# Kernel optimization log

Hardware: AMD Instinct MI355X
Metric: run time of the kernel (lower is better)

## Reference

```python
import jax, jax.numpy as jnp
import numpy as np

B, C, H, W = 8, 384, 32, 32
NH, DK, DV = 8, 48, 48
CFF = 4 * C
L = H * W
NBIAS = (2 * H - 1) * (2 * W - 1)
LN_EPS = 1e-5


def _relative_indices(height, width):
    # rel_idx[q, k] = (gy_k - gy_q + H) * W + (gx_k - gx_q + W), matching the torch loop
    gy, gx = np.meshgrid(np.arange(height), np.arange(width), indexing='ij')
    gy = gy.ravel(); gx = gx.ravel()
    rel = (gy[None, :] - gy[:, None] + height) * width + (gx[None, :] - gx[:, None] + width)
    return jnp.asarray(rel, dtype=jnp.int64)


def setup_inputs() -> dict:
    key = jax.random.key(0)
    ks = jax.random.split(key, 10)
    s = 0.02  # small init scale
    return {
        'x': jax.random.normal(ks[0], (B, C, H, W), dtype=jnp.float32),
        'gamma': jnp.ones((C,), jnp.float32),
        'beta': jnp.zeros((C,), jnp.float32),
        'Wq': jax.random.normal(ks[1], (NH * DK, C), jnp.float32) * s,
        'Wk': jax.random.normal(ks[2], (NH * DK, C), jnp.float32) * s,
        'Wv': jax.random.normal(ks[3], (NH * DV, C), jnp.float32) * s,
        'Wo': jax.random.normal(ks[4], (C, NH * DV), jnp.float32) * s,
        'bo': jnp.zeros((C,), jnp.float32),
        'rel_bias': jax.random.normal(ks[5], (NH, NBIAS), jnp.float32),
        'fc1_w': jax.random.normal(ks[6], (CFF, C), jnp.float32) * s,
        'fc1_b': jnp.zeros((CFF,), jnp.float32),
        'fc2_w': jax.random.normal(ks[7], (C, CFF), jnp.float32) * s,
        'fc2_b': jnp.zeros((C,), jnp.float32),
        'rel_idx': _relative_indices(H, W),
    }


def reference(x, gamma, beta, Wq, Wk, Wv, Wo, bo, rel_bias,
              fc1_w, fc1_b, fc2_w, fc2_b, rel_idx):
    b, c, h_sp, w_sp = x.shape
    l = h_sp * w_sp
    nh = rel_bias.shape[0]
    dk = Wq.shape[0] // nh
    dv = Wv.shape[0] // nh

    # LayerNorm over channel dim (NHWC), then flatten to tokens [b, l, c]
    t = jnp.transpose(x, (0, 2, 3, 1))
    mu = jnp.mean(t, axis=-1, keepdims=True)
    var = jnp.mean(jnp.square(t - mu), axis=-1, keepdims=True)
    t = (t - mu) / jnp.sqrt(var + LN_EPS) * gamma + beta
    tok = t.reshape(b, l, c)

    q = (tok @ Wq.T).reshape(b, l, nh, dk)
    k = (tok @ Wk.T).reshape(b, l, nh, dk)
    v = (tok @ Wv.T).reshape(b, l, nh, dv)

    # gathered relative position bias: [nh, l, l]
    bias = rel_bias[:, rel_idx]
    # note: original applies NO 1/sqrt(d_k) scaling
    scores = jnp.einsum('blhd,bmhd->bhlm', q, k) + bias[None]
    attn = jax.nn.softmax(scores, axis=-1)
    out = jnp.einsum('bhlm,bmhd->blhd', attn, v).reshape(b, l, nh * dv)
    out = out @ Wo.T + bo  # [b, l, c]
    out = jnp.transpose(out, (0, 2, 1)).reshape(b, c, h_sp, w_sp)

    y = x + out  # attention residual (x_stem = x, no downsampling)

    # FFN: 1x1 convs == per-pixel linear over channels; exact (erf) gelu as torch default
    u = jnp.einsum('bchw,oc->bohw', y, fc1_w) + fc1_b[None, :, None, None]
    u = jax.nn.gelu(u, approximate=False)
    u = jnp.einsum('bchw,oc->bohw', u, fc2_w) + fc2_b[None, :, None, None]
    return y + u
```

## Files before the change

kernel.cpp:

```cpp
#include <hip/hip_runtime.h>
#include <math.h>

#define SL 1024
#define CH 384
#define NHEAD 8
#define DH 48
#define NBIAS 3969
#define NTOK 8192
#define BATCH 8
#define CFF 1536
#define LN_EPS 1e-5f
#define QKVLD 1152
#define HMS 3145728
#define LOG2E 1.4426950408889634f

#define WQKV_OFF 0
#define WO_OFF   442368
#define F1_OFF   589824
#define F2_OFF   1179648
#define WTOT     1769472

typedef float floatx4 __attribute__((ext_vector_type(4)));
typedef short bf16x8 __attribute__((ext_vector_type(8)));

__device__ __forceinline__ unsigned f2bf_u(float f) {
  unsigned u = __float_as_uint(f);
  return (u + 0x7fffu + ((u >> 16) & 1u)) >> 16;
}
__device__ __forceinline__ unsigned pack2(float a, float b) {
  return f2bf_u(a) | (f2bf_u(b) << 16);
}

__device__ __forceinline__ void gload_lds16(const void* g, void* l) {
  __builtin_amdgcn_global_load_lds(
      (const __attribute__((address_space(1))) void*)g,
      (__attribute__((address_space(3))) void*)l, 16, 0, 0);
}

__global__ void k_w2bf(const float* __restrict__ Wq, const float* __restrict__ Wk,
                       const float* __restrict__ Wv, const float* __restrict__ Wo,
                       const float* __restrict__ f1, const float* __restrict__ f2,
                       short* __restrict__ dst) {
  size_t i = ((size_t)blockIdx.x * 256 + threadIdx.x) * 8;
  if (i >= WTOT) return;
  const float* s;
  size_t base;
  if (i < 147456)        { s = Wq; base = 0; }
  else if (i < 294912)   { s = Wk; base = 147456; }
  else if (i < WO_OFF)   { s = Wv; base = 294912; }
  else if (i < F1_OFF)   { s = Wo; base = WO_OFF; }
  else if (i < F2_OFF)   { s = f1; base = F1_OFF; }
  else                   { s = f2; base = F2_OFF; }
  const float4* p = (const float4*)(s + (i - base));
  float4 a = p[0], b = p[1];
  uint4 o;
  o.x = pack2(a.x, a.y); o.y = pack2(a.z, a.w);
  o.z = pack2(b.x, b.y); o.w = pack2(b.z, b.w);
  *(uint4*)(dst + i) = o;
}

__global__ __launch_bounds__(256) void k_ln_fused(
    const float* __restrict__ x, const float* __restrict__ gamma,
    const float* __restrict__ beta, short* __restrict__ tok) {
  __shared__ float sx[32][385];
  int b = blockIdx.y, l0 = blockIdx.x * 32;
  int tid = threadIdx.x;
  const float* xb = x + (size_t)b * CH * SL;
  int cr = tid >> 3, ls = (tid & 7) * 4;
#pragma unroll
  for (int c0 = 0; c0 < CH; c0 += 32) {
    int c = c0 + cr;
    float4 v = *(const float4*)(xb + (size_t)c * SL + l0 + ls);
    sx[ls + 0][c] = v.x; sx[ls + 1][c] = v.y;
    sx[ls + 2][c] = v.z; sx[ls + 3][c] = v.w;
  }
  __syncthreads();
  int tl = tid >> 3, p = tid & 7;
  float vals[48];
  float s = 0.f, q = 0.f;
#pragma unroll
  for (int i = 0; i < 48; i++) {
    float v = sx[tl][p * 48 + i];
    vals[i] = v; s += v; q += v * v;
  }
  s += __shfl_xor(s, 1, 64); q += __shfl_xor(q, 1, 64);
  s += __shfl_xor(s, 2, 64); q += __shfl_xor(q, 2, 64);
  s += __shfl_xor(s, 4, 64); q += __shfl_xor(q, 4, 64);
  float mu = s * (1.0f / CH);
  float rstd = rsqrtf(q * (1.0f / CH) - mu * mu + LN_EPS);
  short* orow = tok + (size_t)(b * SL + l0 + tl) * CH + p * 48;
#pragma unroll
  for (int i = 0; i < 48; i += 2) {
    float a = (vals[i] - mu) * rstd * gamma[p * 48 + i] + beta[p * 48 + i];
    float c = (vals[i + 1] - mu) * rstd * gamma[p * 48 + i + 1] + beta[p * 48 + i + 1];
    *(unsigned*)(orow + i) = pack2(a, c);
  }
}

template <int BM, bool GELU, bool HAS_BIAS, int RES_MODE, int OUT_MODE>
__global__ __launch_bounds__(256) void k_gemm_mfma(
    const short* __restrict__ A, const short* __restrict__ W,
    const float* __restrict__ bias, const float* __restrict__ res,
    float* __restrict__ Cf, short* __restrict__ Cb, float* __restrict__ Ct,
    short* __restrict__ Chm, int N, int K) {
  constexpr int MI = BM / 32;
  constexpr int ASI = BM * 2 / 64;
  __shared__ short As[BM * 64];
  __shared__ short Bs[128 * 64];
  int tid = threadIdx.x;
  int wid = tid >> 6, lane = tid & 63;
  int lanelo = lane & 15, quad = lane >> 4;
  int wm = wid & 1, wn = wid >> 1;
  int m0 = blockIdx.y * BM, n0 = blockIdx.x * 128;

  const short* Aga[ASI];
  short* Ala[ASI];
#pragma unroll
  for (int s = 0; s < ASI; s++) {
    int p = wid * (BM * 2) + s * 64 + lane;
    int row = p >> 3, ch = (p & 7) ^ (row & 7);
    Aga[s] = A + (size_t)(m0 + row) * K + ch * 8;
    Ala[s] = As + (wid * (BM * 2) + s * 64) * 8;
  }
  const short* Bga[4];
  short* Bla[4];
#pragma unroll
  for (int s = 0; s < 4; s++) {
    int p = wid * 256 + s * 64 + lane;
    int row = p >> 3, ch = (p & 7) ^ (row & 7);
    Bga[s] = W + (size_t)(n0 + row) * K + ch * 8;
    Bla[s] = Bs + (wid * 256 + s * 64) * 8;
  }

  floatx4 acc[MI][4];
#pragma unroll
  for (int i = 0; i < MI; i++)
#pragma unroll
    for (int j = 0; j < 4; j++) acc[i][j] = {0.f, 0.f, 0.f, 0.f};

  int x8 = lanelo & 7;
  int ca0 = (quad ^ x8) * 8;
  int ca1 = ((quad + 4) ^ x8) * 8;

  for (int k0 = 0; k0 < K; k0 += 64) {
    __syncthreads();
#pragma unroll
    for (int s = 0; s < ASI; s++) gload_lds16(Aga[s] + k0, Ala[s]);
#pragma unroll
    for (int s = 0; s < 4; s++) gload_lds16(Bga[s] + k0, Bla[s]);
    __syncthreads();
#pragma unroll
    for (int h = 0; h < 2; h++) {
      int co = h ? ca1 : ca0;
      bf16x8 af[MI], bq[4];
#pragma unroll
      for (int i = 0; i < MI; i++)
        af[i] = *(const bf16x8*)&As[(wm * (BM / 2) + i * 16 + lanelo) * 64 + co];
#pragma unroll
      for (int j = 0; j < 4; j++)
        bq[j] = *(const bf16x8*)&Bs[(wn * 64 + j * 16 + lanelo) * 64 + co];
#pragma unroll
      for (int i = 0; i < MI; i++)
#pragma unroll
        for (int j = 0; j < 4; j++)
          acc[i][j] = __builtin_amdgcn_mfma_f32_16x16x32_bf16(af[i], bq[j], acc[i][j], 0, 0, 0);
    }
  }

  int colb = n0 + wn * 64 + lanelo;
  float bvv[4];
#pragma unroll
  for (int j = 0; j < 4; j++) bvv[j] = HAS_BIAS ? bias[colb + j * 16] : 0.0f;
#pragma unroll
  for (int i = 0; i < MI; i++) {
    int r = m0 + wm * (BM / 2) + i * 16 + quad * 4;
    int bb = r >> 10, ll = r & 1023;
#pragma unroll
    for (int j = 0; j < 4; j++) {
      int c = colb + j * 16;
      float4 rv = {0.f, 0.f, 0.f, 0.f};
      if (RES_MODE == 2) rv = *(const float4*)(res + ((size_t)bb * CH + c) * SL + ll);
      float vv[4];
#pragma unroll
      for (int reg = 0; reg < 4; reg++) {
        float v = acc[i][j][reg] + bvv[j];
        if (RES_MODE == 1) v += res[(size_t)(r + reg) * N + c];
        if (RES_MODE == 2) v += (&rv.x)[reg];
        if (GELU) v = 0.5f * v * (1.0f + erff(v * 0.7071067811865476f));
        vv[reg] = v;
      }
      if (OUT_MODE & 1) {
#pragma unroll
        for (int reg = 0; reg < 4; reg++) Cf[(size_t)(r + reg) * N + c] = vv[reg];
      }
      if (OUT_MODE & 2) {
#pragma unroll
        for (int reg = 0; reg < 4; reg++) Cb[(size_t)(r + reg) * N + c] = (short)f2bf_u(vv[reg]);
      }
      if (OUT_MODE & 4) {
        float4 ov = {vv[0], vv[1], vv[2], vv[3]};
        *(float4*)(Ct + ((size_t)bb * CH + c) * SL + ll) = ov;
      }
      if (OUT_MODE & 8) {
        int part = c / 384;
        int rem = c - part * 384;
        int hh = rem / 48, dd = rem - hh * 48;
        short* dst = Chm + (size_t)part * HMS +
                     ((size_t)(bb * NHEAD + hh) * SL + ll) * 48 + dd;
#pragma unroll
        for (int reg = 0; reg < 4; reg++) dst[reg * 48] = (short)f2bf_u(vv[reg]);
      }
    }
  }
}

__global__ __launch_bounds__(256) void k_attn_mfma(
    const short* __restrict__ qh, const short* __restrict__ kh,
    const short* __restrict__ vh, const float* __restrict__ rel_bias,
    short* __restrict__ ao) {
  __shared__ short QP[128 * 72];
  __shared__ short Ks[64 * 72];
  __shared__ short Vts[48 * 72];
  __shared__ float Bb[1152];

  int b = blockIdx.z, h = blockIdx.y;
  int l0 = blockIdx.x * 128;
  int tid = threadIdx.x;
  int wid = tid >> 6, lane = tid & 63;
  int lanelo = lane & 15, quad = lane >> 4;
  size_t hb = ((size_t)b * NHEAD + h) * SL;
  size_t bSL = (size_t)b * SL;
  const short* kbase = kh + hb * 48;
  const short* vbase = vh + hb * 48;

  {
    const short* qsrc = qh + (hb + l0) * 48;
#pragma unroll
    for (int s = 0; s < 3; s++) {
      int g = tid + 256 * s;
      int row = g / 6, pos = g - row * 6;
      *(uint4*)&QP[row * 72 + pos * 8] = *(const uint4*)(qsrc + g * 8);
    }
  }
  {
    const float* bsrc = rel_bias + h * NBIAS + (929 - l0);
    for (int j = tid; j < 1152; j += 256) Bb[j] = bsrc[j] * LOG2E;
  }
  for (int z = tid; z < 128 * 8; z += 256) {
    int r = z >> 3, u = z & 7;
    ((unsigned*)&QP[r * 72 + 48])[u] = 0u;
    if (r < 64) ((unsigned*)&Ks[r * 72 + 48])[u] = 0u;
  }
  __syncthreads();

  bf16x8 aq[2][2];
#pragma unroll
  for (int qi = 0; qi < 2; qi++) {
    aq[qi][0] = *(const bf16x8*)&QP[(wid * 32 + qi * 16 + lanelo) * 72 + quad * 8];
    aq[qi][1] = *(const bf16x8*)&QP[(wid * 32 + qi * 16 + lanelo) * 72 + 32 + quad * 8];
  }

  floatx4 O[3][2];
#pragma unroll
  for (int dt = 0; dt < 3; dt++)
#pragma unroll
    for (int qi = 0; qi < 2; qi++) O[dt][qi] = {0.f, 0.f, 0.f, 0.f};
  float lsum[2] = {0.f, 0.f};
  int boff[2];
#pragma unroll
  for (int qi = 0; qi < 2; qi++)
    boff[qi] = 127 + quad * 4 - (wid * 32 + qi * 16 + lanelo);

  int kg = 2 * tid;
  int krow = kg / 6, kpos = kg - krow * 6;
  int vmp = tid & 31, vdg = tid >> 5;
  int kk = 2 * vmp;
  int vcol = (kk & 3) + ((kk >> 2) & 3) * 8 + ((kk >> 4) & 1) * 4 + (kk >> 5) * 32;

  for (int mt = 0; mt < SL; mt += 64) {
    __syncthreads();
    if (tid < 192) {
      const short* ksrc = kbase + (size_t)mt * 48 + kg * 8;
      *(uint4*)&Ks[krow * 72 + kpos * 8] = *(const uint4*)(ksrc);
      *(uint4*)&Ks[krow * 72 + (kpos + 1) * 8] = *(const uint4*)(ksrc + 8);
      const short* vs = vbase + (size_t)(mt + kk) * 48 + vdg * 8;
      union { uint4 u; unsigned short s[8]; } va, vb;
      va.u = *(const uint4*)vs;
      vb.u = *(const uint4*)(vs + 48);
#pragma unroll
      for (int i = 0; i < 8; i++) {
        unsigned pk = (unsigned)va.s[i] | ((unsigned)vb.s[i] << 16);
        *(unsigned*)&Vts[(vdg * 8 + i) * 72 + vcol] = pk;
      }
    }
    __syncthreads();

    bf16x8 kb[4][2];
#pragma unroll
    for (int nt = 0; nt < 4; nt++) {
      kb[nt][0] = *(const bf16x8*)&Ks[(nt * 16 + lanelo) * 72 + quad * 8];
      kb[nt][1] = *(const bf16x8*)&Ks[(nt * 16 + lanelo) * 72 + 32 + quad * 8];
    }
    bf16x8 vf[3][2];
#pragma unroll
    for (int dt = 0; dt < 3; dt++) {
      vf[dt][0] = *(const bf16x8*)&Vts[(dt * 16 + lanelo) * 72 + quad * 8];
      vf[dt][1] = *(const bf16x8*)&Vts[(dt * 16 + lanelo) * 72 + 32 + quad * 8];
    }

#pragma unroll
    for (int qi = 0; qi < 2; qi++) {
      floatx4 sc[4];
#pragma unroll
      for (int nt = 0; nt < 4; nt++) {
        floatx4 a = {0.f, 0.f, 0.f, 0.f};
        a = __builtin_amdgcn_mfma_f32_16x16x32_bf16(kb[nt][0], aq[qi][0], a, 0, 0, 0);
        a = __builtin_amdgcn_mfma_f32_16x16x32_bf16(kb[nt][1], aq[qi][1], a, 0, 0, 0);
        sc[nt] = a;
      }
      unsigned pw[4][2];
#pragma unroll
      for (int nt = 0; nt < 4; nt++) {
        int bidx = boff[qi] + mt + nt * 16;
        float e0 = exp2f(fmaf(sc[nt][0], LOG2E, Bb[bidx + 0]));
        float e1 = exp2f(fmaf(sc[nt][1], LOG2E, Bb[bidx + 1]));
        float e2 = exp2f(fmaf(sc[nt][2], LOG2E, Bb[bidx + 2]));
        float e3 = exp2f(fmaf(sc[nt][3], LOG2E, Bb[bidx + 3]));
        lsum[qi] += (e0 + e1) + (e2 + e3);
        pw[nt][0] = pack2(e0, e1);
        pw[nt][1] = pack2(e2, e3);
      }
      union U8 { unsigned u[4]; bf16x8 v; };
      U8 pb0, pb1;
      pb0.u[0] = pw[0][0]; pb0.u[1] = pw[0][1]; pb0.u[2] = pw[1][0]; pb0.u[3] = pw[1][1];
      pb1.u[0] = pw[2][0]; pb1.u[1] = pw[2][1]; pb1.u[2] = pw[3][0]; pb1.u[3] = pw[3][1];
#pragma unroll
      for (int dt = 0; dt < 3; dt++) {
        O[dt][qi] = __builtin_amdgcn_mfma_f32_16x16x32_bf16(vf[dt][0], pb0.v, O[dt][qi], 0, 0, 0);
        O[dt][qi] = __builtin_amdgcn_mfma_f32_16x16x32_bf16(vf[dt][1], pb1.v, O[dt][qi], 0, 0, 0);
      }
    }
  }

  float inv[2];
#pragma unroll
  for (int qi = 0; qi < 2; qi++) {
    float s = lsum[qi];
    s += __shfl_xor(s, 16, 64);
    s += __shfl_xor(s, 32, 64);
    inv[qi] = 1.0f / s;
  }
#pragma unroll
  for (int dt = 0; dt < 3; dt++)
#pragma unroll
    for (int qi = 0; qi < 2; qi++) {
      unsigned w0 = pack2(O[dt][qi][0] * inv[qi], O[dt][qi][1] * inv[qi]);
      unsigned w1 = pack2(O[dt][qi][2] * inv[qi], O[dt][qi][3] * inv[qi]);
      uint2 wv = {w0, w1};
      *(uint2*)&QP[(wid * 32 + qi * 16 + lanelo) * 72 + dt * 16 + quad * 4] = wv;
    }
  __asm__ volatile("s_waitcnt lgkmcnt(0)" ::: "memory");
#pragma unroll
  for (int s = 0; s < 3; s++) {
    int g = lane + 64 * s;
    int qloc = g / 6, pos = g - qloc * 6;
    uint4 val = *(const uint4*)&QP[(wid * 32 + qloc) * 72 + pos * 8];
    *(uint4*)(ao + (bSL + (size_t)(l0 + wid * 32 + qloc)) * CH + h * DH + pos * 8) = val;
  }
}

extern "C" void kernel_launch(void* const* d_in, const int* in_sizes, int n_in,
                              void* d_out, int out_size, void* d_ws, size_t ws_size,
                              hipStream_t stream) {
  const float* x = (const float*)d_in[0];
  const float* gamma = (const float*)d_in[1];
  const float* beta = (const float*)d_in[2];
  const float* Wq = (const float*)d_in[3];
  const float* Wk = (const float*)d_in[4];
  const float* Wv = (const float*)d_in[5];
  const float* Wo = (const float*)d_in[6];
  const float* bo = (const float*)d_in[7];
  const float* rel_bias = (const float*)d_in[8];
  const float* fc1_w = (const float*)d_in[9];
  const float* fc1_b = (const float*)d_in[10];
  const float* fc2_w = (const float*)d_in[11];
  const float* fc2_b = (const float*)d_in[12];
  float* out = (float*)d_out;

  const size_t TOKCH = (size_t)NTOK * CH;
  float* ws_f = (float*)d_ws;
  float* yb = ws_f;
  short* wbf    = (short*)(yb + TOKCH);
  short* tok_bf = wbf + WTOT;
  short* hm     = tok_bf + TOKCH;
  short* ao_bf  = hm + 3 * (size_t)HMS;
  short* yb_bf  = ao_bf + TOKCH;
  short* h1_bf  = yb_bf + TOKCH;

  k_w2bf<<<WTOT / 8 / 256, 256, 0, stream>>>(Wq, Wk, Wv, Wo, fc1_w, fc2_w, wbf);
  k_ln_fused<<<dim3(SL / 32, BATCH), 256, 0, stream>>>(x, gamma, beta, tok_bf);

  k_gemm_mfma<128, false, false, 0, 8>
      <<<dim3(QKVLD / 128, NTOK / 128), 256, 0, stream>>>(
          tok_bf, wbf + WQKV_OFF, nullptr, nullptr, nullptr, nullptr, nullptr,
          hm, QKVLD, CH);

  k_attn_mfma<<<dim3(SL / 128, NHEAD, BATCH), 256, 0, stream>>>(
      hm, hm + HMS, hm + 2 * (size_t)HMS, rel_bias, ao_bf);

  k_gemm_mfma<64, false, true, 2, 3>
      <<<dim3(CH / 128, NTOK / 64), 256, 0, stream>>>(
          ao_bf, wbf + WO_OFF, bo, x, yb, yb_bf, nullptr, nullptr, CH, CH);

  k_gemm_mfma<128, true, true, 0, 2>
      <<<dim3(CFF / 128, NTOK / 128), 256, 0, stream>>>(
          yb_bf, wbf + F1_OFF, fc1_b, nullptr, nullptr, h1_bf, nullptr, nullptr,
          CFF, CH);

  k_gemm_mfma<64, false, true, 1, 4>
      <<<dim3(CH / 128, NTOK / 64), 256, 0, stream>>>(
          h1_bf, wbf + F2_OFF, fc2_b, yb, nullptr, nullptr, out, nullptr, CH, CFF);
}
```

Before: 215.4 us.

## Double-buffer K/V tiles in attention and use hardware exp2/bf16 pack instructions

```diff
diff --git a/kernel.cpp b/kernel.cpp
--- a/kernel.cpp
+++ b/kernel.cpp
@@ -29,6 +29,11 @@
 }
 __device__ __forceinline__ unsigned pack2(float a, float b) {
   return f2bf_u(a) | (f2bf_u(b) << 16);
+}
+__device__ __forceinline__ unsigned cvtpk(float lo, float hi) {
+  unsigned r;
+  asm("v_cvt_pk_bf16_f32 %0, %1, %2" : "=v"(r) : "v"(lo), "v"(hi));
+  return r;
 }
 
 __device__ __forceinline__ void gload_lds16(const void* g, void* l) {
@@ -219,9 +224,9 @@
     const short* __restrict__ vh, const float* __restrict__ rel_bias,
     short* __restrict__ ao) {
   __shared__ short QP[128 * 72];
-  __shared__ short Ks[64 * 72];
-  __shared__ short Vts[48 * 72];
-  __shared__ float Bb[1152];
+  __shared__ short Ks[2][64 * 72];
+  __shared__ short Vts[2][48 * 72];
+  float* Bb = (float*)QP;
 
   int b = blockIdx.z, h = blockIdx.y;
   int l0 = blockIdx.x * 128;
@@ -242,14 +247,13 @@
       *(uint4*)&QP[row * 72 + pos * 8] = *(const uint4*)(qsrc + g * 8);
     }
   }
-  {
-    const float* bsrc = rel_bias + h * NBIAS + (929 - l0);
-    for (int j = tid; j < 1152; j += 256) Bb[j] = bsrc[j] * LOG2E;
-  }
   for (int z = tid; z < 128 * 8; z += 256) {
     int r = z >> 3, u = z & 7;
     ((unsigned*)&QP[r * 72 + 48])[u] = 0u;
-    if (r < 64) ((unsigned*)&Ks[r * 72 + 48])[u] = 0u;
+    if (r < 64) {
+      ((unsigned*)&Ks[0][r * 72 + 48])[u] = 0u;
+      ((unsigned*)&Ks[1][r * 72 + 48])[u] = 0u;
+    }
   }
   __syncthreads();
 
@@ -259,53 +263,76 @@
     aq[qi][0] = *(const bf16x8*)&QP[(wid * 32 + qi * 16 + lanelo) * 72 + quad * 8];
     aq[qi][1] = *(const bf16x8*)&QP[(wid * 32 + qi * 16 + lanelo) * 72 + 32 + quad * 8];
   }
-
-  floatx4 O[3][2];
-#pragma unroll
-  for (int dt = 0; dt < 3; dt++)
-#pragma unroll
-    for (int qi = 0; qi < 2; qi++) O[dt][qi] = {0.f, 0.f, 0.f, 0.f};
-  float lsum[2] = {0.f, 0.f};
-  int boff[2];
-#pragma unroll
-  for (int qi = 0; qi < 2; qi++)
-    boff[qi] = 127 + quad * 4 - (wid * 32 + qi * 16 + lanelo);
+  __syncthreads();
 
   int kg = 2 * tid;
   int krow = kg / 6, kpos = kg - krow * 6;
   int vmp = tid & 31, vdg = tid >> 5;
   int kk = 2 * vmp;
   int vcol = (kk & 3) + ((kk >> 2) & 3) * 8 + ((kk >> 4) & 1) * 4 + (kk >> 5) * 32;
-
+  unsigned sel_e = 0x05040100u, sel_o = 0x07060302u;
+
+  {
+    const float* bsrc = rel_bias + h * NBIAS + (929 - l0);
+    for (int j = tid; j < 1152; j += 256) Bb[j] = bsrc[j] * LOG2E;
+  }
+  if (tid < 192) {
+    const short* ksrc = kbase + kg * 8;
+    uint4 k0 = *(const uint4*)(ksrc);
+    uint4 k1 = *(const uint4*)(ksrc + 8);
+    const short* vs = vbase + (size_t)kk * 48 + vdg * 8;
+    uint4 va = *(const uint4*)vs;
+    uint4 vb = *(const uint4*)(vs + 48);
+    *(uint4*)&Ks[0][krow * 72 + kpos * 8] = k0;
+    *(uint4*)&Ks[0][krow * 72 + (kpos + 1) * 8] = k1;
+#pragma unroll
+    for (int j = 0; j < 4; j++) {
+      unsigned wa = ((const unsigned*)&va)[j], wb = ((const unsigned*)&vb)[j];
+      unsigned pe, po;
+      asm("v_perm_b32 %0, %1, %2, %3" : "=v"(pe) : "v"(wb), "v"(wa), "v"(sel_e));
+      asm("v_perm_b32 %0, %1, %2, %3" : "=v"(po) : "v"(wb), "v"(wa), "v"(sel_o));
+      *(unsigned*)&Vts[0][(vdg * 8 + 2 * j + 0) * 72 + vcol] = pe;
+      *(unsigned*)&Vts[0][(vdg * 8 + 2 * j + 1) * 72 + vcol] = po;
+    }
+  }
+  __syncthreads();
+
+  floatx4 O[3][2];
+#pragma unroll
+  for (int dt = 0; dt < 3; dt++)
+#pragma unroll
+    for (int qi = 0; qi < 2; qi++) O[dt][qi] = {0.f, 0.f, 0.f, 0.f};
+  float lsum[2] = {0.f, 0.f};
+  int boff[2];
+#pragma unroll
+  for (int qi = 0; qi < 2; qi++)
+    boff[qi] = 127 + quad * 4 - (wid * 32 + qi * 16 + lanelo);
+
+  int cur = 0;
   for (int mt = 0; mt < SL; mt += 64) {
-    __syncthreads();
+    bool last = (mt + 64 >= SL);
+    int mtn = last ? 0 : mt + 64;
+    uint4 k0n, k1n, van, vbn;
     if (tid < 192) {
-      const short* ksrc = kbase + (size_t)mt * 48 + kg * 8;
-      *(uint4*)&Ks[krow * 72 + kpos * 8] = *(const uint4*)(ksrc);
-      *(uint4*)&Ks[krow * 72 + (kpos + 1) * 8] = *(const uint4*)(ksrc + 8);
-      const short* vs = vbase + (size_t)(mt + kk) * 48 + vdg * 8;
-      union { uint4 u; unsigned short s[8]; } va, vb;
-      va.u = *(const uint4*)vs;
-      vb.u = *(const uint4*)(vs + 48);
-#pragma unroll
-      for (int i = 0; i < 8; i++) {
-        unsigned pk = (unsigned)va.s[i] | ((unsigned)vb.s[i] << 16);
-        *(unsigned*)&Vts[(vdg * 8 + i) * 72 + vcol] = pk;
-      }
-    }
-    __syncthreads();
+      const short* ksrc = kbase + (size_t)mtn * 48 + kg * 8;
+      k0n = *(const uint4*)(ksrc);
+      k1n = *(const uint4*)(ksrc + 8);
+      const short* vs = vbase + (size_t)(mtn + kk) * 48 + vdg * 8;
+      van = *(const uint4*)vs;
+      vbn = *(const uint4*)(vs + 48);
+    }
 
     bf16x8 kb[4][2];
 #pragma unroll
     for (int nt = 0; nt < 4; nt++) {
-      kb[nt][0] = *(const bf16x8*)&Ks[(nt * 16 + lanelo) * 72 + quad * 8];
-      kb[nt][1] = *(const bf16x8*)&Ks[(nt * 16 + lanelo) * 72 + 32 + quad * 8];
+      kb[nt][0] = *(const bf16x8*)&Ks[cur][(nt * 16 + lanelo) * 72 + quad * 8];
+      kb[nt][1] = *(const bf16x8*)&Ks[cur][(nt * 16 + lanelo) * 72 + 32 + quad * 8];
     }
     bf16x8 vf[3][2];
 #pragma unroll
     for (int dt = 0; dt < 3; dt++) {
-      vf[dt][0] = *(const bf16x8*)&Vts[(dt * 16 + lanelo) * 72 + quad * 8];
-      vf[dt][1] = *(const bf16x8*)&Vts[(dt * 16 + lanelo) * 72 + 32 + quad * 8];
+      vf[dt][0] = *(const bf16x8*)&Vts[cur][(dt * 16 + lanelo) * 72 + quad * 8];
+      vf[dt][1] = *(const bf16x8*)&Vts[cur][(dt * 16 + lanelo) * 72 + 32 + quad * 8];
     }
 
 #pragma unroll
@@ -318,44 +345,62 @@
         a = __builtin_amdgcn_mfma_f32_16x16x32_bf16(kb[nt][1], aq[qi][1], a, 0, 0, 0);
         sc[nt] = a;
       }
-      unsigned pw[4][2];
+      union U8 { unsigned u[4]; bf16x8 v; };
+      U8 pb0, pb1;
 #pragma unroll
       for (int nt = 0; nt < 4; nt++) {
         int bidx = boff[qi] + mt + nt * 16;
-        float e0 = exp2f(fmaf(sc[nt][0], LOG2E, Bb[bidx + 0]));
-        float e1 = exp2f(fmaf(sc[nt][1], LOG2E, Bb[bidx + 1]));
-        float e2 = exp2f(fmaf(sc[nt][2], LOG2E, Bb[bidx + 2]));
-        float e3 = exp2f(fmaf(sc[nt][3], LOG2E, Bb[bidx + 3]));
+        float e0 = __builtin_amdgcn_exp2f(fmaf(sc[nt][0], LOG2E, Bb[bidx + 0]));
+        float e1 = __builtin_amdgcn_exp2f(fmaf(sc[nt][1], LOG2E, Bb[bidx + 1]));
+        float e2 = __builtin_amdgcn_exp2f(fmaf(sc[nt][2], LOG2E, Bb[bidx + 2]));
+        float e3 = __builtin_amdgcn_exp2f(fmaf(sc[nt][3], LOG2E, Bb[bidx + 3]));
         lsum[qi] += (e0 + e1) + (e2 + e3);
-        pw[nt][0] = pack2(e0, e1);
-        pw[nt][1] = pack2(e2, e3);
-      }
-      union U8 { unsigned u[4]; bf16x8 v; };
-      U8 pb0, pb1;
-      pb0.u[0] = pw[0][0]; pb0.u[1] = pw[0][1]; pb0.u[2] = pw[1][0]; pb0.u[3] = pw[1][1];
-      pb1.u[0] = pw[2][0]; pb1.u[1] = pw[2][1]; pb1.u[2] = pw[3][0]; pb1.u[3] = pw[3][1];
+        unsigned p01 = cvtpk(e0, e1), p23 = cvtpk(e2, e3);
+        if (nt == 0) { pb0.u[0] = p01; pb0.u[1] = p23; }
+        else if (nt == 1) { pb0.u[2] = p01; pb0.u[3] = p23; }
+        else if (nt == 2) { pb1.u[0] = p01; pb1.u[1] = p23; }
+        else { pb1.u[2] = p01; pb1.u[3] = p23; }
+      }
 #pragma unroll
       for (int dt = 0; dt < 3; dt++) {
         O[dt][qi] = __builtin_amdgcn_mfma_f32_16x16x32_bf16(vf[dt][0], pb0.v, O[dt][qi], 0, 0, 0);
         O[dt][qi] = __builtin_amdgcn_mfma_f32_16x16x32_bf16(vf[dt][1], pb1.v, O[dt][qi], 0, 0, 0);
       }
     }
-  }
-
+
+    if (tid < 192 && !last) {
+      int nxt = cur ^ 1;
+      *(uint4*)&Ks[nxt][krow * 72 + kpos * 8] = k0n;
+      *(uint4*)&Ks[nxt][krow * 72 + (kpos + 1) * 8] = k1n;
+#pragma unroll
+      for (int j = 0; j < 4; j++) {
+        unsigned wa = ((const unsigned*)&van)[j], wb = ((const unsigned*)&vbn)[j];
+        unsigned pe, po;
+        asm("v_perm_b32 %0, %1, %2, %3" : "=v"(pe) : "v"(wb), "v"(wa), "v"(sel_e));
+        asm("v_perm_b32 %0, %1, %2, %3" : "=v"(po) : "v"(wb), "v"(wa), "v"(sel_o));
+        *(unsigned*)&Vts[nxt][(vdg * 8 + 2 * j + 0) * 72 + vcol] = pe;
+        *(unsigned*)&Vts[nxt][(vdg * 8 + 2 * j + 1) * 72 + vcol] = po;
+      }
+    }
+    __syncthreads();
+    cur ^= 1;
+  }
+
+  __syncthreads();
   float inv[2];
 #pragma unroll
   for (int qi = 0; qi < 2; qi++) {
     float s = lsum[qi];
     s += __shfl_xor(s, 16, 64);
     s += __shfl_xor(s, 32, 64);
-    inv[qi] = 1.0f / s;
+    inv[qi] = __builtin_amdgcn_rcpf(s);
   }
 #pragma unroll
   for (int dt = 0; dt < 3; dt++)
 #pragma unroll
     for (int qi = 0; qi < 2; qi++) {
-      unsigned w0 = pack2(O[dt][qi][0] * inv[qi], O[dt][qi][1] * inv[qi]);
-      unsigned w1 = pack2(O[dt][qi][2] * inv[qi], O[dt][qi][3] * inv[qi]);
+      unsigned w0 = cvtpk(O[dt][qi][0] * inv[qi], O[dt][qi][1] * inv[qi]);
+      unsigned w1 = cvtpk(O[dt][qi][2] * inv[qi], O[dt][qi][3] * inv[qi]);
       uint2 wv = {w0, w1};
       *(uint2*)&QP[(wid * 32 + qi * 16 + lanelo) * 72 + dt * 16 + quad * 4] = wv;
     }
```

Measured after the change: 201.4 us. 6.5% less time.
